# Kernel optimization log

Hardware: AMD Instinct MI355X
Metric: run time of the kernel (lower is better)

The kernel has to match this reference:

```python
import jax, jax.numpy as jnp
import numpy as np

B, S = 4096, 64
L, W = 16, 8          # fixed letter image size in the module
K = 3                 # kernel size
OL, OW = L - K + 1, W - K + 1  # 14, 6 (valid conv, stride 1)


def setup_inputs() -> dict:
    key = jax.random.key(0)
    k1, k2 = jax.random.split(key)
    x = jax.random.normal(k1, (B, S, L * W), dtype=jnp.float32)
    kernel = jax.random.normal(k2, (K, K), dtype=jnp.float32)
    return {"x": x, "kernel": kernel}


def reference(x, kernel):
    # x: [B, S, 128] -> images [B*S, 1, 16, 8]
    imgs = x.reshape(B * S, 1, L, W)
    kern = kernel.reshape(1, 1, K, K)  # OIHW
    out = jax.lax.conv_general_dilated(
        imgs, kern,
        window_strides=(1, 1), padding="VALID",
        dimension_numbers=("NCHW", "OIHW", "NCHW"),
    )  # [B*S, 1, 14, 6]
    out = out.reshape(B, S, OL * OW)
    return jax.nn.relu(out)
```

## Files before the change

kernel.cpp:

```cpp
#include <hip/hip_runtime.h>


#define BLOCK 256
#define IPB   64
#define STRIDE 132
#define NC    4
#define NIMG_TOTAL (4096 * 64)

__global__ __launch_bounds__(BLOCK, 4) void conv3x3_relu_kernel(
    const float* __restrict__ x,
    const float* __restrict__ kern,
    float* __restrict__ out)
{
    __shared__ float s[IPB * STRIDE];

    const int tid = threadIdx.x;
    const float k00 = kern[0], k01 = kern[1], k02 = kern[2];
    const float k10 = kern[3], k11 = kern[4], k12 = kern[5];
    const float k20 = kern[6], k21 = kern[7], k22 = kern[8];

    const int img  = tid >> 2;
    const int tq   = tid & 3;
    const int rs   = (tq < 2) ? (tq * 4) : (8 + (tq - 2) * 3);
    const int rcnt = (tq < 2) ? 4 : 3;

    const long long base_img = (long long)blockIdx.x * (IPB * NC);

    float4 pf[2][8];

    {
        const float4* src = reinterpret_cast<const float4*>(x + base_img * 128);
        #pragma unroll
        for (int it = 0; it < 8; ++it) pf[0][it] = src[it * BLOCK + tid];
    }

    #pragma unroll
    for (int t = 0; t < NC; ++t) {
        if (t > 0) __syncthreads();

        #pragma unroll
        for (int it = 0; it < 8; ++it) {
            const int f  = it * BLOCK + tid;
            const int im = f >> 5;
            const int o4 = f & 31;
            *reinterpret_cast<float4*>(&s[im * STRIDE + o4 * 4]) = pf[t & 1][it];
        }

        if (t + 1 < NC) {
            const float4* src = reinterpret_cast<const float4*>(
                x + (base_img + (long long)(t + 1) * IPB) * 128);
            #pragma unroll
            for (int it = 0; it < 8; ++it) pf[(t + 1) & 1][it] = src[it * BLOCK + tid];
        }
        __syncthreads();

        const float* ip = &s[img * STRIDE];
        float w[3][8];
        float acc[4][6];
        *reinterpret_cast<float4*>(&w[0][0]) = *reinterpret_cast<const float4*>(ip + rs * 8);
        *reinterpret_cast<float4*>(&w[0][4]) = *reinterpret_cast<const float4*>(ip + rs * 8 + 4);
        *reinterpret_cast<float4*>(&w[1][0]) = *reinterpret_cast<const float4*>(ip + (rs + 1) * 8);
        *reinterpret_cast<float4*>(&w[1][4]) = *reinterpret_cast<const float4*>(ip + (rs + 1) * 8 + 4);
        #pragma unroll
        for (int rr = 0; rr < 4; ++rr) {
            if (rr < rcnt) {
                float* wn = w[(rr + 2) % 3];
                *reinterpret_cast<float4*>(&wn[0]) =
                    *reinterpret_cast<const float4*>(ip + (rs + rr + 2) * 8);
                *reinterpret_cast<float4*>(&wn[4]) =
                    *reinterpret_cast<const float4*>(ip + (rs + rr + 2) * 8 + 4);
                const float* r0 = w[rr % 3];
                const float* r1 = w[(rr + 1) % 3];
                const float* r2 = wn;
                #pragma unroll
                for (int c = 0; c < 6; ++c) {
                    float a = r0[c] * k00 + r0[c + 1] * k01 + r0[c + 2] * k02
                            + r1[c] * k10 + r1[c + 1] * k11 + r1[c + 2] * k12
                            + r2[c] * k20 + r2[c + 1] * k21 + r2[c + 2] * k22;
                    acc[rr][c] = fmaxf(a, 0.0f);
                }
            }
        }
        __syncthreads();

        #pragma unroll
        for (int rr = 0; rr < 4; ++rr) {
            if (rr < rcnt) {
                float* op = &s[img * 84 + (rs + rr) * 6];
                *reinterpret_cast<float2*>(op)     = make_float2(acc[rr][0], acc[rr][1]);
                *reinterpret_cast<float2*>(op + 2) = make_float2(acc[rr][2], acc[rr][3]);
                *reinterpret_cast<float2*>(op + 4) = make_float2(acc[rr][4], acc[rr][5]);
            }
        }
        __syncthreads();

        float4* dst = reinterpret_cast<float4*>(
            out + (base_img + (long long)t * IPB) * 84);
        const float4* s4 = reinterpret_cast<const float4*>(s);
        #pragma unroll
        for (int it = 0; it < 6; ++it) {
            const int f = it * BLOCK + tid;
            if (f < (IPB * 84) / 4) dst[f] = s4[f];
        }
    }
}

extern "C" void kernel_launch(void* const* d_in, const int* in_sizes, int n_in,
                              void* d_out, int out_size, void* d_ws, size_t ws_size,
                              hipStream_t stream) {
    const float* x    = (const float*)d_in[0];
    const float* kern = (const float*)d_in[1];
    float* out        = (float*)d_out;
    const int nblocks = NIMG_TOTAL / (IPB * NC);
    conv3x3_relu_kernel<<<nblocks, BLOCK, 0, stream>>>(x, kern, out);
}
```

Before: 241.8 us.

## Give each wavefront its own LDS slice and drop block barriers

Restructures the kernel so each 64-lane wavefront independently loads, convolves and stores 16 images in a private LDS slice. Block-wide __syncthreads are replaced by lgkmcnt waits plus wave barriers. The block now processes one chunk of 64 images, so the grid is four times larger, and the register double-buffered prefetch across chunks is removed. Global loads and stores become nontemporal. This trades explicit software pipelining for more independent waves and less synchronization.

```diff
diff --git a/kernel.cpp b/kernel.cpp
--- a/kernel.cpp
+++ b/kernel.cpp
@@ -2,106 +2,106 @@
 
 
 #define BLOCK 256
-#define IPB   64
+#define IPW   16
 #define STRIDE 132
-#define NC    4
+#define SLICE (IPW * STRIDE)
 #define NIMG_TOTAL (4096 * 64)
+
+typedef float f32x4 __attribute__((ext_vector_type(4)));
+typedef float f32x2 __attribute__((ext_vector_type(2)));
+
+#define FENCE_LDS() do { \
+    asm volatile("s_waitcnt lgkmcnt(0)" ::: "memory"); \
+    __builtin_amdgcn_wave_barrier(); \
+} while (0)
 
 __global__ __launch_bounds__(BLOCK, 4) void conv3x3_relu_kernel(
     const float* __restrict__ x,
     const float* __restrict__ kern,
     float* __restrict__ out)
 {
-    __shared__ float s[IPB * STRIDE];
+    __shared__ float s[4 * SLICE];
 
-    const int tid = threadIdx.x;
+    const int tid  = threadIdx.x;
+    const int wid  = tid >> 6;
+    const int lane = tid & 63;
+    float* sw = &s[wid * SLICE];
+
     const float k00 = kern[0], k01 = kern[1], k02 = kern[2];
     const float k10 = kern[3], k11 = kern[4], k12 = kern[5];
     const float k20 = kern[6], k21 = kern[7], k22 = kern[8];
 
-    const int img  = tid >> 2;
-    const int tq   = tid & 3;
-    const int rs   = (tq < 2) ? (tq * 4) : (8 + (tq - 2) * 3);
-    const int rcnt = (tq < 2) ? 4 : 3;
+    const long long imgbase = (long long)blockIdx.x * 64 + wid * IPW;
 
-    const long long base_img = (long long)blockIdx.x * (IPB * NC);
-
-    float4 pf[2][8];
-
-    {
-        const float4* src = reinterpret_cast<const float4*>(x + base_img * 128);
-        #pragma unroll
-        for (int it = 0; it < 8; ++it) pf[0][it] = src[it * BLOCK + tid];
-    }
+    const f32x4* src = reinterpret_cast<const f32x4*>(x) + imgbase * 32;
+    f32x4 pf[8];
+    #pragma unroll
+    for (int k = 0; k < 8; ++k)
+        pf[k] = __builtin_nontemporal_load(&src[k * 64 + lane]);
 
     #pragma unroll
-    for (int t = 0; t < NC; ++t) {
-        if (t > 0) __syncthreads();
+    for (int k = 0; k < 8; ++k) {
+        const int f  = k * 64 + lane;
+        const int im = f >> 5;
+        const int o4 = f & 31;
+        *reinterpret_cast<f32x4*>(&sw[im * STRIDE + o4 * 4]) = pf[k];
+    }
+    FENCE_LDS();
 
-        #pragma unroll
-        for (int it = 0; it < 8; ++it) {
-            const int f  = it * BLOCK + tid;
-            const int im = f >> 5;
-            const int o4 = f & 31;
-            *reinterpret_cast<float4*>(&s[im * STRIDE + o4 * 4]) = pf[t & 1][it];
-        }
+    const int img  = lane >> 2;
+    const int tq   = lane & 3;
+    const int rs   = tq * 4 - (tq >> 1);
+    const int rcnt = 4 - (tq & 1);
+    const float* ip = &sw[img * STRIDE];
 
-        if (t + 1 < NC) {
-            const float4* src = reinterpret_cast<const float4*>(
-                x + (base_img + (long long)(t + 1) * IPB) * 128);
+    float w[3][8];
+    float acc[4][6];
+    *reinterpret_cast<f32x4*>(&w[0][0]) = *reinterpret_cast<const f32x4*>(ip + rs * 8);
+    *reinterpret_cast<f32x4*>(&w[0][4]) = *reinterpret_cast<const f32x4*>(ip + rs * 8 + 4);
+    *reinterpret_cast<f32x4*>(&w[1][0]) = *reinterpret_cast<const f32x4*>(ip + (rs + 1) * 8);
+    *reinterpret_cast<f32x4*>(&w[1][4]) = *reinterpret_cast<const f32x4*>(ip + (rs + 1) * 8 + 4);
+    #pragma unroll
+    for (int rr = 0; rr < 4; ++rr) {
+        if (rr < rcnt) {
+            float* wn = w[(rr + 2) % 3];
+            *reinterpret_cast<f32x4*>(&wn[0]) =
+                *reinterpret_cast<const f32x4*>(ip + (rs + rr + 2) * 8);
+            *reinterpret_cast<f32x4*>(&wn[4]) =
+                *reinterpret_cast<const f32x4*>(ip + (rs + rr + 2) * 8 + 4);
+            const float* r0 = w[rr % 3];
+            const float* r1 = w[(rr + 1) % 3];
+            const float* r2 = wn;
             #pragma unroll
-            for (int it = 0; it < 8; ++it) pf[(t + 1) & 1][it] = src[it * BLOCK + tid];
-        }
-        __syncthreads();
-
-        const float* ip = &s[img * STRIDE];
-        float w[3][8];
-        float acc[4][6];
-        *reinterpret_cast<float4*>(&w[0][0]) = *reinterpret_cast<const float4*>(ip + rs * 8);
-        *reinterpret_cast<float4*>(&w[0][4]) = *reinterpret_cast<const float4*>(ip + rs * 8 + 4);
-        *reinterpret_cast<float4*>(&w[1][0]) = *reinterpret_cast<const float4*>(ip + (rs + 1) * 8);
-        *reinterpret_cast<float4*>(&w[1][4]) = *reinterpret_cast<const float4*>(ip + (rs + 1) * 8 + 4);
-        #pragma unroll
-        for (int rr = 0; rr < 4; ++rr) {
-            if (rr < rcnt) {
-                float* wn = w[(rr + 2) % 3];
-                *reinterpret_cast<float4*>(&wn[0]) =
-                    *reinterpret_cast<const float4*>(ip + (rs + rr + 2) * 8);
-                *reinterpret_cast<float4*>(&wn[4]) =
-                    *reinterpret_cast<const float4*>(ip + (rs + rr + 2) * 8 + 4);
-                const float* r0 = w[rr % 3];
-                const float* r1 = w[(rr + 1) % 3];
-                const float* r2 = wn;
-                #pragma unroll
-                for (int c = 0; c < 6; ++c) {
-                    float a = r0[c] * k00 + r0[c + 1] * k01 + r0[c + 2] * k02
-                            + r1[c] * k10 + r1[c + 1] * k11 + r1[c + 2] * k12
-                            + r2[c] * k20 + r2[c + 1] * k21 + r2[c + 2] * k22;
-                    acc[rr][c] = fmaxf(a, 0.0f);
-                }
+            for (int c = 0; c < 6; ++c) {
+                float a = r0[c] * k00 + r0[c + 1] * k01 + r0[c + 2] * k02
+                        + r1[c] * k10 + r1[c + 1] * k11 + r1[c + 2] * k12
+                        + r2[c] * k20 + r2[c + 1] * k21 + r2[c + 2] * k22;
+                acc[rr][c] = fmaxf(a, 0.0f);
             }
         }
-        __syncthreads();
+    }
+    FENCE_LDS();
 
-        #pragma unroll
-        for (int rr = 0; rr < 4; ++rr) {
-            if (rr < rcnt) {
-                float* op = &s[img * 84 + (rs + rr) * 6];
-                *reinterpret_cast<float2*>(op)     = make_float2(acc[rr][0], acc[rr][1]);
-                *reinterpret_cast<float2*>(op + 2) = make_float2(acc[rr][2], acc[rr][3]);
-                *reinterpret_cast<float2*>(op + 4) = make_float2(acc[rr][4], acc[rr][5]);
-            }
+    #pragma unroll
+    for (int rr = 0; rr < 4; ++rr) {
+        if (rr < rcnt) {
+            float* op = &sw[img * 84 + (rs + rr) * 6];
+            f32x2 v01; v01.x = acc[rr][0]; v01.y = acc[rr][1];
+            f32x2 v23; v23.x = acc[rr][2]; v23.y = acc[rr][3];
+            f32x2 v45; v45.x = acc[rr][4]; v45.y = acc[rr][5];
+            *reinterpret_cast<f32x2*>(op)     = v01;
+            *reinterpret_cast<f32x2*>(op + 2) = v23;
+            *reinterpret_cast<f32x2*>(op + 4) = v45;
         }
-        __syncthreads();
+    }
+    FENCE_LDS();
 
-        float4* dst = reinterpret_cast<float4*>(
-            out + (base_img + (long long)t * IPB) * 84);
-        const float4* s4 = reinterpret_cast<const float4*>(s);
-        #pragma unroll
-        for (int it = 0; it < 6; ++it) {
-            const int f = it * BLOCK + tid;
-            if (f < (IPB * 84) / 4) dst[f] = s4[f];
-        }
+    f32x4* dst = reinterpret_cast<f32x4*>(out + imgbase * 84);
+    const f32x4* s4 = reinterpret_cast<const f32x4*>(sw);
+    #pragma unroll
+    for (int k = 0; k < 6; ++k) {
+        const int f = k * 64 + lane;
+        if (f < 336) __builtin_nontemporal_store(s4[f], &dst[f]);
     }
 }
 
@@ -111,6 +111,6 @@
     const float* x    = (const float*)d_in[0];
     const float* kern = (const float*)d_in[1];
     float* out        = (float*)d_out;
-    const int nblocks = NIMG_TOTAL / (IPB * NC);
+    const int nblocks = NIMG_TOTAL / 64;
     conv3x3_relu_kernel<<<nblocks, BLOCK, 0, stream>>>(x, kern, out);
 }
```

Result: faster. 206.7 us (-14.5%).
